# Performance work log

Measured on AMD Instinct MI355X. Metric: run time of the kernel, lower is better.

Reference implementation:

```python
import jax, jax.numpy as jnp
import numpy as np

MARGIN = 0.2
EPS = 1e-6  # torch.pairwise_distance adds eps to the difference before the norm


def setup_inputs() -> dict:
    key = jax.random.key(0)
    k1, k2, k3 = jax.random.split(key, 3)
    B, D = 8192, 128
    emb1 = jax.random.normal(k1, (B, D), dtype=jnp.float32)
    emb2 = jax.random.normal(k2, (B, D), dtype=jnp.float32)
    target = jax.random.randint(k3, (B,), 0, 2, dtype=jnp.int64)
    return {"emb1": emb1, "emb2": emb2, "target": target}


def reference(emb1, emb2, target):
    B, D = emb1.shape
    # torch.pairwise_distance(a, b) = ||a - b + EPS||_2; expand the square:
    # |a-b+eps|^2 = |a|^2 + |b|^2 - 2 a.b + 2*eps*(sum(a)-sum(b)) + D*eps^2
    sq = (
        jnp.sum(emb1 * emb1, axis=-1)[:, None]
        + jnp.sum(emb2 * emb2, axis=-1)[None, :]
        - 2.0 * (emb1 @ emb2.T)
        + 2.0 * EPS * (jnp.sum(emb1, axis=-1)[:, None] - jnp.sum(emb2, axis=-1)[None, :])
        + D * EPS * EPS
    )
    dist = jnp.sqrt(jnp.maximum(sq, 0.0))  # [B, B]: dist[i, j] = ||emb1[i] - emb2[j] + eps||

    pos = target == 1
    neg = target == 0
    # hardest positive: max over columns j with target[j]==1; hardest negative: min over target[j]==0
    pos_max = jnp.max(jnp.where(pos[None, :], dist, -jnp.inf), axis=1)  # [B]
    neg_min = jnp.min(jnp.where(neg[None, :], dist, jnp.inf), axis=1)   # [B]
    per_anchor = jnp.maximum(pos_max - neg_min + MARGIN, 0.0)
    anchor_w = pos.astype(dist.dtype)
    # mean over anchors (rows i with target[i]==1)
    return jnp.sum(per_anchor * anchor_w) / jnp.sum(anchor_w)
```

## Files before the change

### kernel.cpp

```cpp
#include <hip/hip_runtime.h>
#include <hip/hip_bf16.h>
#include <math.h>


#define DDIM   128
#define SPLITS 8
#define MARGIN 0.2f
#define EPS    1e-6f
#define SENT   1e30f

#define CHUNK_PITCH 1056
#define WAVE_SPAN   (8 * CHUNK_PITCH)
#define TILE_BYTES  (4 * WAVE_SPAN)

typedef unsigned short ushort_t;
typedef __attribute__((ext_vector_type(8))) short short8;
typedef __attribute__((ext_vector_type(4))) float f32x4;

__device__ __forceinline__ ushort_t f2bf(float f) {
    unsigned int u = __float_as_uint(f);
    u = (u + 0x7FFFu + ((u >> 16) & 1u)) >> 16;
    return (ushort_t)u;
}

__device__ __forceinline__ void g2lds16(const ushort_t* g, void* lds) {
    __builtin_amdgcn_global_load_lds(
        (const __attribute__((address_space(1))) unsigned int*)g,
        (__attribute__((address_space(3))) unsigned int*)lds,
        16, 0, 0);
}

__global__ void prep_kernel(const float* __restrict__ e1, const float* __restrict__ e2,
                            const int* __restrict__ target,
                            ushort_t* __restrict__ e1b, ushort_t* __restrict__ e2b,
                            float* __restrict__ rowterm,
                            float* __restrict__ cpos, float* __restrict__ cneg,
                            float* __restrict__ redsum, int* __restrict__ ticket, int B) {
    if (blockIdx.x == 0 && threadIdx.x == 0) {
        redsum[0] = 0.f; redsum[1] = 0.f; *ticket = 0;
    }
    int w    = (blockIdx.x * blockDim.x + threadIdx.x) >> 6;
    int lane = threadIdx.x & 63;
    if (w >= 2 * B) return;
    bool first = (w < B);
    int r = first ? w : w - B;
    const float* src = (first ? e1 : e2) + (size_t)r * DDIM;
    float2 v = *(const float2*)(src + lane * 2);
    ushort_t* dst = (first ? e1b : e2b) + (size_t)r * DDIM;
    ushort2 o; o.x = f2bf(v.x); o.y = f2bf(v.y);
    *(ushort2*)(dst + lane * 2) = o;
    float s = v.x + v.y;
    float n = v.x * v.x + v.y * v.y;
    #pragma unroll
    for (int off = 32; off > 0; off >>= 1) {
        s += __shfl_down(s, off, 64);
        n += __shfl_down(n, off, 64);
    }
    if (lane == 0) {
        if (first) {
            rowterm[r] = n + 2.f * EPS * s + (float)DDIM * EPS * EPS;
        } else {
            float ct = n - 2.f * EPS * s;
            int tg = target[r];
            cpos[r] = (tg == 1) ? ct : -SENT;
            cneg[r] = (tg == 0) ? ct :  SENT;
        }
    }
}

__device__ __forceinline__ void stage_tile_dma(const ushort_t* __restrict__ gRow0,
                                               unsigned char* __restrict__ lds,
                                               int w, int l) {
    const ushort_t* g = gRow0 + (size_t)(w * 32) * DDIM + l * 8;
    unsigned char* lp = lds + w * WAVE_SPAN;
    #pragma unroll
    for (int it = 0; it < 8; ++it)
        g2lds16(g + it * 512, lp + it * CHUNK_PITCH);
}

__global__ __launch_bounds__(256, 2)
void tile_kernel(const ushort_t* __restrict__ e1b, const ushort_t* __restrict__ e2b,
                 const float* __restrict__ cpos, const float* __restrict__ cneg,
                 float* __restrict__ pmp, float* __restrict__ nmp, int B) {
    __shared__ __align__(16) unsigned char As[TILE_BYTES];
    __shared__ __align__(16) unsigned char Bs[TILE_BYTES];

    const int tid = threadIdx.x;
    const int w   = tid >> 6;
    const int l   = tid & 63;
    const int lq  = l >> 4;
    const int lm  = l & 15;
    const int row0 = blockIdx.x * 128;
    const int colSpan = B / SPLITS;
    const int col0 = blockIdx.y * colSpan;
    const int nTiles = colSpan / 128;

    const int wr = (w >> 1) * 64;
    const int wc = (w & 1) * 64;

    const unsigned char* aLane = As + ((wr >> 2) + (lm >> 2)) * CHUNK_PITCH
                                    + (lm & 3) * 256 + lq * 16;
    const unsigned char* bLane = Bs + ((wc >> 2) + (lm >> 2)) * CHUNK_PITCH
                                    + (lm & 3) * 256 + lq * 16;

    stage_tile_dma(e1b + (size_t)row0 * DDIM, As, w, l);
    stage_tile_dma(e2b + (size_t)col0 * DDIM, Bs, w, l);
    __syncthreads();

    short8 afr[4][4];
    #pragma unroll
    for (int i = 0; i < 4; ++i)
        #pragma unroll
        for (int k4 = 0; k4 < 4; ++k4)
            afr[i][k4] = *(const short8*)(aLane + i * (4 * CHUNK_PITCH) + k4 * 64);

    float pm[4][4], nm[4][4];
    #pragma unroll
    for (int i = 0; i < 4; ++i)
        #pragma unroll
        for (int r = 0; r < 4; ++r) { pm[i][r] = -SENT; nm[i][r] = SENT; }

    for (int t = 0; t < nTiles; ++t) {
        f32x4 acc[4][4];
        #pragma unroll
        for (int i = 0; i < 4; ++i)
            #pragma unroll
            for (int j = 0; j < 4; ++j)
                acc[i][j] = (f32x4){0.f, 0.f, 0.f, 0.f};

        #pragma unroll
        for (int kk = 0; kk < DDIM; kk += 32) {
            const int k4 = kk >> 5;
            const int ko = kk * 2;
            short8 bf[4];
            #pragma unroll
            for (int j = 0; j < 4; ++j)
                bf[j] = *(const short8*)(bLane + j * (4 * CHUNK_PITCH) + ko);
            #pragma unroll
            for (int i = 0; i < 4; ++i)
                #pragma unroll
                for (int j = 0; j < 4; ++j)
                    acc[i][j] = __builtin_amdgcn_mfma_f32_16x16x32_bf16(
                                    afr[i][k4], bf[j], acc[i][j], 0, 0, 0);
        }

        #pragma unroll
        for (int j = 0; j < 4; ++j) {
            int col = col0 + t * 128 + wc + j * 16 + lm;
            float cp = cpos[col];
            float cn = cneg[col];
            #pragma unroll
            for (int i = 0; i < 4; ++i)
                #pragma unroll
                for (int r = 0; r < 4; ++r) {
                    float d = acc[i][j][r];
                    pm[i][r] = fmaxf(pm[i][r], fmaf(-2.f, d, cp));
                    nm[i][r] = fminf(nm[i][r], fmaf(-2.f, d, cn));
                }
        }

        if (t + 1 < nTiles) {
            __syncthreads();
            stage_tile_dma(e2b + (size_t)(col0 + (t + 1) * 128) * DDIM, Bs, w, l);
            __syncthreads();
        }
    }

    #pragma unroll
    for (int m = 1; m < 16; m <<= 1) {
        #pragma unroll
        for (int i = 0; i < 4; ++i)
            #pragma unroll
            for (int r = 0; r < 4; ++r) {
                pm[i][r] = fmaxf(pm[i][r], __shfl_xor(pm[i][r], m, 64));
                nm[i][r] = fminf(nm[i][r], __shfl_xor(nm[i][r], m, 64));
            }
    }

    __syncthreads();
    float* smP = (float*)As;
    float* smN = smP + 128;
    if ((w & 1) == 1 && lm == 0) {
        #pragma unroll
        for (int i = 0; i < 4; ++i)
            #pragma unroll
            for (int r = 0; r < 4; ++r) {
                int lr = wr + i * 16 + lq * 4 + r;
                smP[lr] = pm[i][r];
                smN[lr] = nm[i][r];
            }
    }
    __syncthreads();
    if ((w & 1) == 0 && lm == 0) {
        #pragma unroll
        for (int i = 0; i < 4; ++i)
            #pragma unroll
            for (int r = 0; r < 4; ++r) {
                int lr  = wr + i * 16 + lq * 4 + r;
                int row = row0 + lr;
                pmp[(size_t)blockIdx.y * B + row] = fmaxf(pm[i][r], smP[lr]);
                nmp[(size_t)blockIdx.y * B + row] = fminf(nm[i][r], smN[lr]);
            }
    }
}

__global__ void reduce_kernel(const float* __restrict__ pmp, const float* __restrict__ nmp,
                              const float* __restrict__ rowterm, const int* __restrict__ target,
                              float* __restrict__ redsum, int* __restrict__ ticket,
                              float* __restrict__ out, int B) {
    int row = blockIdx.x * blockDim.x + threadIdx.x;
    float s = 0.f, c = 0.f;
    {
        float pmv = -SENT, nmv = SENT;
        #pragma unroll
        for (int sp = 0; sp < SPLITS; ++sp) {
            pmv = fmaxf(pmv, pmp[(size_t)sp * B + row]);
            nmv = fminf(nmv, nmp[(size_t)sp * B + row]);
        }
        float rt = rowterm[row];
        float dp = sqrtf(fmaxf(rt + pmv, 0.f));
        float dn = sqrtf(fmaxf(rt + nmv, 0.f));
        if (target[row] == 1) {
            s = fmaxf(dp - dn + MARGIN, 0.f);
            c = 1.f;
        }
    }
    #pragma unroll
    for (int off = 32; off > 0; off >>= 1) {
        s += __shfl_down(s, off, 64);
        c += __shfl_down(c, off, 64);
    }
    __shared__ float ls[4], lc[4];
    int wv = threadIdx.x >> 6, ln = threadIdx.x & 63;
    if (ln == 0) { ls[wv] = s; lc[wv] = c; }
    __syncthreads();
    if (threadIdx.x == 0) {
        float ss = ls[0] + ls[1] + ls[2] + ls[3];
        float cc = lc[0] + lc[1] + lc[2] + lc[3];
        atomicAdd(&redsum[0], ss);
        atomicAdd(&redsum[1], cc);
        __threadfence();
        int done = atomicAdd(ticket, 1);
        if (done == (int)gridDim.x - 1) {
            __threadfence();
            float fs = __hip_atomic_load(&redsum[0], __ATOMIC_RELAXED, __HIP_MEMORY_SCOPE_AGENT);
            float fc = __hip_atomic_load(&redsum[1], __ATOMIC_RELAXED, __HIP_MEMORY_SCOPE_AGENT);
            out[0] = fs / fc;
        }
    }
}

extern "C" void kernel_launch(void* const* d_in, const int* in_sizes, int n_in,
                              void* d_out, int out_size, void* d_ws, size_t ws_size,
                              hipStream_t stream) {
    const float* e1     = (const float*)d_in[0];
    const float* e2     = (const float*)d_in[1];
    const int*   target = (const int*)d_in[2];
    float* out = (float*)d_out;
    const int B = in_sizes[2];

    char* p = (char*)d_ws;
    ushort_t* e1b  = (ushort_t*)p;   p += (size_t)B * DDIM * 2;
    ushort_t* e2b  = (ushort_t*)p;   p += (size_t)B * DDIM * 2;
    float* rowterm = (float*)p;      p += (size_t)B * 4;
    float* cpos    = (float*)p;      p += (size_t)B * 4;
    float* cneg    = (float*)p;      p += (size_t)B * 4;
    float* pmp     = (float*)p;      p += (size_t)SPLITS * B * 4;
    float* nmp     = (float*)p;      p += (size_t)SPLITS * B * 4;
    float* redsum  = (float*)p;      p += 2 * 4;
    int*   ticket  = (int*)p;

    {
        int blocks = (2 * B + 3) / 4;
        prep_kernel<<<blocks, 256, 0, stream>>>(e1, e2, target, e1b, e2b,
                                                rowterm, cpos, cneg, redsum, ticket, B);
    }
    {
        dim3 grid(B / 128, SPLITS);
        tile_kernel<<<grid, 256, 0, stream>>>(e1b, e2b, cpos, cneg, pmp, nmp, B);
    }
    reduce_kernel<<<32, 256, 0, stream>>>(pmp, nmp, rowterm, target,
                                          redsum, ticket, out, B);
}
```

Baseline: 91.40 us.

## Double-buffer B tiles in LDS, load A fragments directly, prescale A by -2

B tiles are now double-buffered in LDS: the next tile is prefetched while the current one is multiplied, leaving one barrier per iteration instead of two. The A fragments are loaded straight from global memory into registers, which frees the LDS used for A. The -2 factor is folded into the bf16 conversion of emb1, so the epilogue uses plain adds with paired max and min chains. Risks are stale reads if a DMA write into a buffer is not ordered against readers of that same buffer, and some extra rounding from prescaling before the bf16 conversion (prescaling by -2 is exact in bf16).

```diff
diff --git a/kernel.cpp b/kernel.cpp
--- a/kernel.cpp
+++ b/kernel.cpp
@@ -47,7 +47,9 @@
     const float* src = (first ? e1 : e2) + (size_t)r * DDIM;
     float2 v = *(const float2*)(src + lane * 2);
     ushort_t* dst = (first ? e1b : e2b) + (size_t)r * DDIM;
-    ushort2 o; o.x = f2bf(v.x); o.y = f2bf(v.y);
+    ushort2 o;
+    if (first) { o.x = f2bf(-2.f * v.x); o.y = f2bf(-2.f * v.y); }
+    else       { o.x = f2bf(v.x);        o.y = f2bf(v.y); }
     *(ushort2*)(dst + lane * 2) = o;
     float s = v.x + v.y;
     float n = v.x * v.x + v.y * v.y;
@@ -82,8 +84,7 @@
 void tile_kernel(const ushort_t* __restrict__ e1b, const ushort_t* __restrict__ e2b,
                  const float* __restrict__ cpos, const float* __restrict__ cneg,
                  float* __restrict__ pmp, float* __restrict__ nmp, int B) {
-    __shared__ __align__(16) unsigned char As[TILE_BYTES];
-    __shared__ __align__(16) unsigned char Bs[TILE_BYTES];
+    __shared__ __align__(16) unsigned char Bs[2][TILE_BYTES];
 
     const int tid = threadIdx.x;
     const int w   = tid >> 6;
@@ -98,29 +99,34 @@
     const int wr = (w >> 1) * 64;
     const int wc = (w & 1) * 64;
 
-    const unsigned char* aLane = As + ((wr >> 2) + (lm >> 2)) * CHUNK_PITCH
-                                    + (lm & 3) * 256 + lq * 16;
-    const unsigned char* bLane = Bs + ((wc >> 2) + (lm >> 2)) * CHUNK_PITCH
-                                    + (lm & 3) * 256 + lq * 16;
-
-    stage_tile_dma(e1b + (size_t)row0 * DDIM, As, w, l);
-    stage_tile_dma(e2b + (size_t)col0 * DDIM, Bs, w, l);
+    const unsigned char* bLane0 = Bs[0] + ((wc >> 2) + (lm >> 2)) * CHUNK_PITCH
+                                        + (lm & 3) * 256 + lq * 16;
+
+    const ushort_t* aG = e1b + (size_t)(row0 + wr + lm) * DDIM + lq * 8;
+    short8 afr[4][4];
+    #pragma unroll
+    for (int i = 0; i < 4; ++i)
+        #pragma unroll
+        for (int k4 = 0; k4 < 4; ++k4)
+            afr[i][k4] = *(const short8*)(aG + i * 16 * DDIM + k4 * 32);
+
+    stage_tile_dma(e2b + (size_t)col0 * DDIM, Bs[0], w, l);
+
+    float pm[4][4], nm[4][4];
+    #pragma unroll
+    for (int i = 0; i < 4; ++i)
+        #pragma unroll
+        for (int r = 0; r < 4; ++r) { pm[i][r] = -SENT; nm[i][r] = SENT; }
+
     __syncthreads();
 
-    short8 afr[4][4];
-    #pragma unroll
-    for (int i = 0; i < 4; ++i)
-        #pragma unroll
-        for (int k4 = 0; k4 < 4; ++k4)
-            afr[i][k4] = *(const short8*)(aLane + i * (4 * CHUNK_PITCH) + k4 * 64);
-
-    float pm[4][4], nm[4][4];
-    #pragma unroll
-    for (int i = 0; i < 4; ++i)
-        #pragma unroll
-        for (int r = 0; r < 4; ++r) { pm[i][r] = -SENT; nm[i][r] = SENT; }
-
     for (int t = 0; t < nTiles; ++t) {
+        if (t + 1 < nTiles)
+            stage_tile_dma(e2b + (size_t)(col0 + (t + 1) * 128) * DDIM,
+                           Bs[(t + 1) & 1], w, l);
+
+        const unsigned char* bl = bLane0 + (t & 1) * TILE_BYTES;
+
         f32x4 acc[4][4];
         #pragma unroll
         for (int i = 0; i < 4; ++i)
@@ -135,7 +141,7 @@
             short8 bf[4];
             #pragma unroll
             for (int j = 0; j < 4; ++j)
-                bf[j] = *(const short8*)(bLane + j * (4 * CHUNK_PITCH) + ko);
+                bf[j] = *(const short8*)(bl + j * (4 * CHUNK_PITCH) + ko);
             #pragma unroll
             for (int i = 0; i < 4; ++i)
                 #pragma unroll
@@ -144,26 +150,26 @@
                                     afr[i][k4], bf[j], acc[i][j], 0, 0, 0);
         }
 
-        #pragma unroll
-        for (int j = 0; j < 4; ++j) {
-            int col = col0 + t * 128 + wc + j * 16 + lm;
-            float cp = cpos[col];
-            float cn = cneg[col];
-            #pragma unroll
-            for (int i = 0; i < 4; ++i)
+        {
+            const int colb = col0 + t * 128 + wc + lm;
+            #pragma unroll
+            for (int jp = 0; jp < 2; ++jp) {
+                const int j0 = 2 * jp, j1 = j0 + 1;
+                const float cp0 = cpos[colb + j0 * 16], cn0 = cneg[colb + j0 * 16];
+                const float cp1 = cpos[colb + j1 * 16], cn1 = cneg[colb + j1 * 16];
                 #pragma unroll
-                for (int r = 0; r < 4; ++r) {
-                    float d = acc[i][j][r];
-                    pm[i][r] = fmaxf(pm[i][r], fmaf(-2.f, d, cp));
-                    nm[i][r] = fminf(nm[i][r], fmaf(-2.f, d, cn));
-                }
-        }
-
-        if (t + 1 < nTiles) {
-            __syncthreads();
-            stage_tile_dma(e2b + (size_t)(col0 + (t + 1) * 128) * DDIM, Bs, w, l);
-            __syncthreads();
-        }
+                for (int i = 0; i < 4; ++i)
+                    #pragma unroll
+                    for (int r = 0; r < 4; ++r) {
+                        const float d0 = acc[i][j0][r];
+                        const float d1 = acc[i][j1][r];
+                        pm[i][r] = fmaxf(fmaxf(pm[i][r], d0 + cp0), d1 + cp1);
+                        nm[i][r] = fminf(fminf(nm[i][r], d0 + cn0), d1 + cn1);
+                    }
+            }
+        }
+
+        __syncthreads();
     }
 
     #pragma unroll
@@ -177,8 +183,7 @@
             }
     }
 
-    __syncthreads();
-    float* smP = (float*)As;
+    float* smP = (float*)Bs;
     float* smN = smP + 128;
     if ((w & 1) == 1 && lm == 0) {
         #pragma unroll
```

Result: no change. 92.67 us (+1.4%).

## Use one 128x128 tile per block with full column split and prescaled bf16

Applied to the files above, without the earlier changes.

The tile kernel now launches one block per 128x128 output tile (64 column splits) instead of looping over 8 column tiles per block. A fragments are loaded straight from global memory into registers, which drops the A LDS buffer and lets occupancy rise to 3 blocks per CU. The -2 scale is folded into emb1 during the bf16 conversion, so the epilogue uses an add instead of an fma. The prep kernel is revectorised to 8 lanes per row with float4 loads. The reduce kernel must now read 64 partials per row, adding partial-result traffic, and each block pays its own staging cost with no overlap.

```diff
diff --git a/kernel.cpp b/kernel.cpp
--- a/kernel.cpp
+++ b/kernel.cpp
@@ -4,7 +4,7 @@
 
 
 #define DDIM   128
-#define SPLITS 8
+#define SPLITS 64
 #define MARGIN 0.2f
 #define EPS    1e-6f
 #define SENT   1e30f
@@ -16,6 +16,7 @@
 typedef unsigned short ushort_t;
 typedef __attribute__((ext_vector_type(8))) short short8;
 typedef __attribute__((ext_vector_type(4))) float f32x4;
+typedef __attribute__((ext_vector_type(4))) unsigned short ushort4_t;
 
 __device__ __forceinline__ ushort_t f2bf(float f) {
     unsigned int u = __float_as_uint(f);
@@ -36,27 +37,35 @@
                             float* __restrict__ rowterm,
                             float* __restrict__ cpos, float* __restrict__ cneg,
                             float* __restrict__ redsum, int* __restrict__ ticket, int B) {
-    if (blockIdx.x == 0 && threadIdx.x == 0) {
-        redsum[0] = 0.f; redsum[1] = 0.f; *ticket = 0;
-    }
-    int w    = (blockIdx.x * blockDim.x + threadIdx.x) >> 6;
-    int lane = threadIdx.x & 63;
-    if (w >= 2 * B) return;
-    bool first = (w < B);
-    int r = first ? w : w - B;
+    if (blockIdx.x == 0) {
+        if (threadIdx.x == 0) { redsum[0] = 0.f; redsum[1] = 0.f; }
+        else if (threadIdx.x == 1) *ticket = 0;
+    }
+    int gr  = blockIdx.x * 32 + (threadIdx.x >> 3);
+    int seg = threadIdx.x & 7;
+    bool first = gr < B;
+    int r = first ? gr : gr - B;
     const float* src = (first ? e1 : e2) + (size_t)r * DDIM;
-    float2 v = *(const float2*)(src + lane * 2);
-    ushort_t* dst = (first ? e1b : e2b) + (size_t)r * DDIM;
-    ushort2 o; o.x = f2bf(v.x); o.y = f2bf(v.y);
-    *(ushort2*)(dst + lane * 2) = o;
-    float s = v.x + v.y;
-    float n = v.x * v.x + v.y * v.y;
-    #pragma unroll
-    for (int off = 32; off > 0; off >>= 1) {
-        s += __shfl_down(s, off, 64);
-        n += __shfl_down(n, off, 64);
-    }
-    if (lane == 0) {
+    ushort_t*    dst = (first ? e1b : e2b) + (size_t)r * DDIM;
+    const float sc = first ? -2.f : 1.f;
+    float s = 0.f, n = 0.f;
+    #pragma unroll
+    for (int it = 0; it < 4; ++it) {
+        int e0 = (seg + it * 8) * 4;
+        float4 v = *(const float4*)(src + e0);
+        ushort4_t o;
+        o.x = f2bf(sc * v.x); o.y = f2bf(sc * v.y);
+        o.z = f2bf(sc * v.z); o.w = f2bf(sc * v.w);
+        *(ushort4_t*)(dst + e0) = o;
+        s += v.x + v.y + v.z + v.w;
+        n += v.x * v.x + v.y * v.y + v.z * v.z + v.w * v.w;
+    }
+    #pragma unroll
+    for (int m = 1; m <= 4; m <<= 1) {
+        s += __shfl_xor(s, m, 64);
+        n += __shfl_xor(n, m, 64);
+    }
+    if (seg == 0) {
         if (first) {
             rowterm[r] = n + 2.f * EPS * s + (float)DDIM * EPS * EPS;
         } else {
@@ -78,11 +87,10 @@
         g2lds16(g + it * 512, lp + it * CHUNK_PITCH);
 }
 
-__global__ __launch_bounds__(256, 2)
+__global__ __launch_bounds__(256, 3)
 void tile_kernel(const ushort_t* __restrict__ e1b, const ushort_t* __restrict__ e2b,
                  const float* __restrict__ cpos, const float* __restrict__ cneg,
                  float* __restrict__ pmp, float* __restrict__ nmp, int B) {
-    __shared__ __align__(16) unsigned char As[TILE_BYTES];
     __shared__ __align__(16) unsigned char Bs[TILE_BYTES];
 
     const int tid = threadIdx.x;
@@ -91,79 +99,60 @@
     const int lq  = l >> 4;
     const int lm  = l & 15;
     const int row0 = blockIdx.x * 128;
-    const int colSpan = B / SPLITS;
-    const int col0 = blockIdx.y * colSpan;
-    const int nTiles = colSpan / 128;
+    const int col0 = blockIdx.y * 128;
 
     const int wr = (w >> 1) * 64;
     const int wc = (w & 1) * 64;
 
-    const unsigned char* aLane = As + ((wr >> 2) + (lm >> 2)) * CHUNK_PITCH
-                                    + (lm & 3) * 256 + lq * 16;
+    stage_tile_dma(e2b + (size_t)col0 * DDIM, Bs, w, l);
+
+    const ushort_t* aG = e1b + (size_t)(row0 + wr + lm) * DDIM + lq * 8;
+    short8 afr[4][4];
+    #pragma unroll
+    for (int i = 0; i < 4; ++i)
+        #pragma unroll
+        for (int k4 = 0; k4 < 4; ++k4)
+            afr[i][k4] = *(const short8*)(aG + i * 16 * DDIM + k4 * 32);
+
     const unsigned char* bLane = Bs + ((wc >> 2) + (lm >> 2)) * CHUNK_PITCH
                                     + (lm & 3) * 256 + lq * 16;
 
-    stage_tile_dma(e1b + (size_t)row0 * DDIM, As, w, l);
-    stage_tile_dma(e2b + (size_t)col0 * DDIM, Bs, w, l);
-    __syncthreads();
-
-    short8 afr[4][4];
+    float pm[4][4], nm[4][4];
     #pragma unroll
     for (int i = 0; i < 4; ++i)
         #pragma unroll
-        for (int k4 = 0; k4 < 4; ++k4)
-            afr[i][k4] = *(const short8*)(aLane + i * (4 * CHUNK_PITCH) + k4 * 64);
-
-    float pm[4][4], nm[4][4];
-    #pragma unroll
-    for (int i = 0; i < 4; ++i)
-        #pragma unroll
         for (int r = 0; r < 4; ++r) { pm[i][r] = -SENT; nm[i][r] = SENT; }
 
-    for (int t = 0; t < nTiles; ++t) {
-        f32x4 acc[4][4];
-        #pragma unroll
-        for (int i = 0; i < 4; ++i)
-            #pragma unroll
-            for (int j = 0; j < 4; ++j)
-                acc[i][j] = (f32x4){0.f, 0.f, 0.f, 0.f};
-
-        #pragma unroll
-        for (int kk = 0; kk < DDIM; kk += 32) {
-            const int k4 = kk >> 5;
-            const int ko = kk * 2;
-            short8 bf[4];
-            #pragma unroll
-            for (int j = 0; j < 4; ++j)
-                bf[j] = *(const short8*)(bLane + j * (4 * CHUNK_PITCH) + ko);
+    __syncthreads();
+
+    #pragma unroll
+    for (int j = 0; j < 4; ++j) {
+        const unsigned char* blj = bLane + j * (4 * CHUNK_PITCH);
+
+        f32x4 acc[4];
+        #pragma unroll
+        for (int i = 0; i < 4; ++i) acc[i] = (f32x4){0.f, 0.f, 0.f, 0.f};
+
+        #pragma unroll
+        for (int k4 = 0; k4 < 4; ++k4) {
+            const short8 bf = *(const short8*)(blj + k4 * 64);
             #pragma unroll
             for (int i = 0; i < 4; ++i)
-                #pragma unroll
-                for (int j = 0; j < 4; ++j)
-                    acc[i][j] = __builtin_amdgcn_mfma_f32_16x16x32_bf16(
-                                    afr[i][k4], bf[j], acc[i][j], 0, 0, 0);
-        }
-
-        #pragma unroll
-        for (int j = 0; j < 4; ++j) {
-            int col = col0 + t * 128 + wc + j * 16 + lm;
-            float cp = cpos[col];
-            float cn = cneg[col];
-            #pragma unroll
-            for (int i = 0; i < 4; ++i)
-                #pragma unroll
-                for (int r = 0; r < 4; ++r) {
-                    float d = acc[i][j][r];
-                    pm[i][r] = fmaxf(pm[i][r], fmaf(-2.f, d, cp));
-                    nm[i][r] = fminf(nm[i][r], fmaf(-2.f, d, cn));
-                }
-        }
-
-        if (t + 1 < nTiles) {
-            __syncthreads();
-            stage_tile_dma(e2b + (size_t)(col0 + (t + 1) * 128) * DDIM, Bs, w, l);
-            __syncthreads();
-        }
+                acc[i] = __builtin_amdgcn_mfma_f32_16x16x32_bf16(
+                             afr[i][k4], bf, acc[i], 0, 0, 0);
+        }
+
+        const int col = col0 + wc + j * 16 + lm;
+        const float cp = cpos[col];
+        const float cn = cneg[col];
+        #pragma unroll
+        for (int i = 0; i < 4; ++i)
+            #pragma unroll
+            for (int r = 0; r < 4; ++r) {
+                const float d = acc[i][r];
+                pm[i][r] = fmaxf(pm[i][r], d + cp);
+                nm[i][r] = fminf(nm[i][r], d + cn);
+            }
     }
 
     #pragma unroll
@@ -177,9 +166,9 @@
             }
     }
 
-    __syncthreads();
-    float* smP = (float*)As;
+    float* smP = (float*)Bs;
     float* smN = smP + 128;
+    __syncthreads();
     if ((w & 1) == 1 && lm == 0) {
         #pragma unroll
         for (int i = 0; i < 4; ++i)
@@ -196,11 +185,15 @@
         for (int i = 0; i < 4; ++i)
             #pragma unroll
             for (int r = 0; r < 4; ++r) {
-                int lr  = wr + i * 16 + lq * 4 + r;
-                int row = row0 + lr;
-                pmp[(size_t)blockIdx.y * B + row] = fmaxf(pm[i][r], smP[lr]);
-                nmp[(size_t)blockIdx.y * B + row] = fminf(nm[i][r], smN[lr]);
-            }
+                int lr = wr + i * 16 + lq * 4 + r;
+                smP[lr] = fmaxf(pm[i][r], smP[lr]);
+                smN[lr] = fminf(nm[i][r], smN[lr]);
+            }
+    }
+    __syncthreads();
+    if (tid < 128) {
+        pmp[(size_t)blockIdx.y * B + row0 + tid] = smP[tid];
+        nmp[(size_t)blockIdx.y * B + row0 + tid] = smN[tid];
     }
 }
 
@@ -212,7 +205,7 @@
     float s = 0.f, c = 0.f;
     {
         float pmv = -SENT, nmv = SENT;
-        #pragma unroll
+        #pragma unroll 8
         for (int sp = 0; sp < SPLITS; ++sp) {
             pmv = fmaxf(pmv, pmp[(size_t)sp * B + row]);
             nmv = fminf(nmv, nmp[(size_t)sp * B + row]);
@@ -271,12 +264,13 @@
     int*   ticket  = (int*)p;
 
     {
-        int blocks = (2 * B + 3) / 4;
+        int blocks = (2 * B) / 32;
         prep_kernel<<<blocks, 256, 0, stream>>>(e1, e2, target, e1b, e2b,
-                                                rowterm, cpos, cneg, redsum, ticket, B);
+                                                rowterm, cpos, cneg,
+                                                redsum, ticket, B);
     }
     {
-        dim3 grid(B / 128, SPLITS);
+        dim3 grid(B / 128, B / 128);
         tile_kernel<<<grid, 256, 0, stream>>>(e1b, e2b, cpos, cneg, pmp, nmp, B);
     }
     reduce_kernel<<<32, 256, 0, stream>>>(pmp, nmp, rowterm, target,
```

After: 119.2 us. 1.3x slower.
